# Kernel tuning notes

Measured on AMD Instinct MI355X. Metric: run time of the kernel, lower is better.

The kernel has to match this reference:

```python
import jax, jax.numpy as jnp
import numpy as np

D_MODEL = 1024
D_FF = 4096
NUM_HEADS = 16
HEAD_DIM = D_MODEL // NUM_HEADS
THETA = 10000.0
EPS = 1e-5


def _trunc_init(key, shape):
    fan_in, fan_out = shape
    sigma = (2.0 / (fan_in + fan_out)) ** 0.5
    return sigma * jax.random.truncated_normal(key, -3.0, 3.0, shape, dtype=jnp.float32)


def setup_inputs() -> dict:
    key = jax.random.key(0)
    ks = jax.random.split(key, 8)
    x = jax.random.normal(ks[0], (2, 2048, D_MODEL), dtype=jnp.float32)
    return {
        "x": x,
        "Wq": _trunc_init(ks[1], (D_MODEL, D_MODEL)),
        "Wk": _trunc_init(ks[2], (D_MODEL, D_MODEL)),
        "Wv": _trunc_init(ks[3], (D_MODEL, D_MODEL)),
        "Wo": _trunc_init(ks[4], (D_MODEL, D_MODEL)),
        "g1": jnp.ones((D_MODEL,), dtype=jnp.float32),
        "g2": jnp.ones((D_MODEL,), dtype=jnp.float32),
        "W1": _trunc_init(ks[5], (D_MODEL, D_FF)),
        "W2": _trunc_init(ks[6], (D_FF, D_MODEL)),
        "W3": _trunc_init(ks[7], (D_MODEL, D_FF)),
    }


def _rmsnorm(x, g):
    xf = x.astype(jnp.float32)
    rms = jnp.sqrt(jnp.mean(xf * xf, axis=-1, keepdims=True) + EPS)
    return (xf / rms * g).astype(x.dtype)


def _rope(x, cos, sin):
    # x: [B, H, S, Dh]; cos/sin: [S, Dh//2]
    x1 = x[..., 0::2]
    x2 = x[..., 1::2]
    o1 = x1 * cos - x2 * sin
    o2 = x2 * cos + x1 * sin
    return jnp.stack([o1, o2], axis=-1).reshape(x.shape)


def reference(x, Wq, Wk, Wv, Wo, g1, g2, W1, W2, W3):
    B, S, _ = x.shape
    # --- attention branch ---
    h = _rmsnorm(x, g1)
    def split_heads(t):
        return t.reshape(B, S, NUM_HEADS, HEAD_DIM).transpose(0, 2, 1, 3)
    Q = split_heads(h @ Wq)
    K = split_heads(h @ Wk)
    V = split_heads(h @ Wv)
    # RoPE
    powers = jnp.arange(0, HEAD_DIM, 2, dtype=jnp.float32) / HEAD_DIM
    inv_freq = 1.0 / (THETA ** powers)
    t = jnp.arange(S, dtype=jnp.float32)
    freqs = jnp.outer(t, inv_freq)  # [S, Dh//2]
    cos, sin = jnp.cos(freqs), jnp.sin(freqs)
    Q = _rope(Q, cos, sin)
    K = _rope(K, cos, sin)
    # scaled dot-product attention with causal mask
    scale = 1.0 / jnp.sqrt(jnp.float32(HEAD_DIM))
    scores = jnp.einsum('bhqd,bhkd->bhqk', Q, K) * scale
    causal = jnp.tril(jnp.ones((S, S), dtype=bool))
    scores = jnp.where(causal, scores, -jnp.inf)
    attn = jax.nn.softmax(scores, axis=-1)
    ctx = jnp.einsum('bhqk,bhkd->bhqd', attn, V)
    ctx = ctx.transpose(0, 2, 1, 3).reshape(B, S, D_MODEL)
    out1 = x + ctx @ Wo
    # --- FFN branch (SwiGLU) ---
    h2 = _rmsnorm(out1, g2)
    x1 = h2 @ W1
    x3 = h2 @ W3
    ffn = (x1 * jax.nn.sigmoid(x1) * x3) @ W2
    return out1 + ffn
```

## Files before the change

kernel.cpp:

```cpp
#include <hip/hip_runtime.h>
#include <math.h>

typedef unsigned short ushort_t;
typedef __attribute__((ext_vector_type(8))) short short8;
typedef __attribute__((ext_vector_type(4))) float f32x4;

#define MFMA16(a, b, c) __builtin_amdgcn_mfma_f32_16x16x32_bf16((a), (b), (c), 0, 0, 0)

static __device__ __forceinline__ float fast_exp2(float x) {
#if __has_builtin(__builtin_amdgcn_exp2f)
  return __builtin_amdgcn_exp2f(x);
#else
  return exp2f(x);
#endif
}

static __device__ __forceinline__ ushort_t f2bf(float f) {
  unsigned int u = __float_as_uint(f);
  u = u + 0x7FFFu + ((u >> 16) & 1u);
  return (ushort_t)(u >> 16);
}
static __device__ __forceinline__ ushort_t f2bf_trunc(float f) {
  return (ushort_t)(__float_as_uint(f) >> 16);
}
static __device__ __forceinline__ float bf2f(ushort_t s) {
  return __uint_as_float(((unsigned int)s) << 16);
}

static __device__ __forceinline__ void stage16(const ushort_t* g_perlane, char* l_uniform, int lane) {
#if __has_builtin(__builtin_amdgcn_global_load_lds)
  __builtin_amdgcn_global_load_lds((const __attribute__((address_space(1))) void*)g_perlane,
                                   (__attribute__((address_space(3))) void*)l_uniform, 16, 0, 0);
#else
  *(uint4*)(l_uniform + lane * 16) = *(const uint4*)g_perlane;
#endif
}

__global__ __launch_bounds__(256) void rmsnorm_k(const float* __restrict__ x,
                                                 const float* __restrict__ g,
                                                 ushort_t* __restrict__ o) {
  const int r = blockIdx.x, t = threadIdx.x;
  const float4 xv = ((const float4*)(x + (size_t)r * 1024))[t];
  float ss = xv.x * xv.x + xv.y * xv.y + xv.z * xv.z + xv.w * xv.w;
#pragma unroll
  for (int m = 32; m >= 1; m >>= 1) ss += __shfl_xor(ss, m);
  __shared__ float wp[4];
  if ((t & 63) == 0) wp[t >> 6] = ss;
  __syncthreads();
  const float inv = rsqrtf((wp[0] + wp[1] + wp[2] + wp[3]) * (1.f / 1024.f) + 1e-5f);
  const float4 gv = ((const float4*)g)[t];
  ushort4 ov = {f2bf(xv.x * inv * gv.x), f2bf(xv.y * inv * gv.y),
                f2bf(xv.z * inv * gv.z), f2bf(xv.w * inv * gv.w)};
  *(ushort4*)(o + (size_t)r * 1024 + t * 4) = ov;
}

__global__ __launch_bounds__(256) void transpose4_k(const float* __restrict__ s0,
                                                    const float* __restrict__ s1,
                                                    const float* __restrict__ s2,
                                                    const float* __restrict__ s3,
                                                    ushort_t* __restrict__ d0,
                                                    ushort_t* __restrict__ d1,
                                                    ushort_t* __restrict__ d2,
                                                    ushort_t* __restrict__ d3) {
  const int z = blockIdx.z;
  const float* in = (z == 0) ? s0 : (z == 1) ? s1 : (z == 2) ? s2 : s3;
  ushort_t* out = (z == 0) ? d0 : (z == 1) ? d1 : (z == 2) ? d2 : d3;
  __shared__ ushort_t Ts[64][72];
  const int t = threadIdx.x;
  const int c0 = blockIdx.x * 64, r0 = blockIdx.y * 64;
  const int lr = t >> 4, lc = (t & 15) * 4;
#pragma unroll
  for (int i = 0; i < 4; ++i) {
    const float4 v = *(const float4*)&in[(size_t)(r0 + lr + i * 16) * 1024 + c0 + lc];
    Ts[lr + i * 16][lc + 0] = f2bf(v.x);
    Ts[lr + i * 16][lc + 1] = f2bf(v.y);
    Ts[lr + i * 16][lc + 2] = f2bf(v.z);
    Ts[lr + i * 16][lc + 3] = f2bf(v.w);
  }
  __syncthreads();
  const int rr = (t & 15) * 4;
#pragma unroll
  for (int i = 0; i < 4; ++i) {
    const int cc = (t >> 4) + i * 16;
    ushort4 o = {Ts[rr + 0][cc], Ts[rr + 1][cc], Ts[rr + 2][cc], Ts[rr + 3][cc]};
    *(ushort4*)&out[(size_t)(c0 + cc) * 1024 + r0 + rr] = o;
  }
}

__global__ __launch_bounds__(256) void transpose3_k(const float* __restrict__ s0,
                                                    const float* __restrict__ s1,
                                                    const float* __restrict__ s2,
                                                    ushort_t* __restrict__ d01,
                                                    ushort_t* __restrict__ d2) {
  const int z = blockIdx.z;
  const float* in;
  ushort_t* out;
  int R, C, mode, c0, r0;
  if (z == 2) {
    in = s2; out = d2; R = 4096; C = 1024; mode = 0;
    const int flat = blockIdx.y * 64 + blockIdx.x;
    c0 = (flat & 15) * 64;
    r0 = (flat >> 4) * 64;
  } else {
    in = (z == 0) ? s0 : s1; out = d01; R = 1024; C = 4096; mode = (z == 0) ? 1 : 2;
    c0 = blockIdx.x * 64;
    r0 = blockIdx.y * 64;
  }
  __shared__ ushort_t Ts[64][72];
  const int t = threadIdx.x;
  const int lr = t >> 4, lc = (t & 15) * 4;
#pragma unroll
  for (int i = 0; i < 4; ++i) {
    const float4 v = *(const float4*)&in[(size_t)(r0 + lr + i * 16) * C + c0 + lc];
    Ts[lr + i * 16][lc + 0] = f2bf(v.x);
    Ts[lr + i * 16][lc + 1] = f2bf(v.y);
    Ts[lr + i * 16][lc + 2] = f2bf(v.z);
    Ts[lr + i * 16][lc + 3] = f2bf(v.w);
  }
  __syncthreads();
  const int rr = (t & 15) * 4;
#pragma unroll
  for (int i = 0; i < 4; ++i) {
    const int cc = (t >> 4) + i * 16;
    const int cg = c0 + cc;
    int orow;
    if (mode == 0)
      orow = cg;
    else
      orow = ((cg >> 7) << 8) + (((cg >> 4) & 7) << 5) + (cg & 15) + (mode == 2 ? 16 : 0);
    ushort4 o = {Ts[rr + 0][cc], Ts[rr + 1][cc], Ts[rr + 2][cc], Ts[rr + 3][cc]};
    *(ushort4*)&out[(size_t)orow * R + r0 + rr] = o;
  }
}

template <int FUSED>
__global__ __launch_bounds__(512, 2) void gemm256_k(const ushort_t* __restrict__ A,
                                                    const ushort_t* __restrict__ Bt,
                                                    ushort_t* __restrict__ C,
                                                    int N, int K) {
  __shared__ uint4 smem[131072 / 16];
  char* sm = (char*)smem;
  const int flat = blockIdx.y * gridDim.x + blockIdx.x;
  const int xcd = flat & 7;
  const int idx = flat >> 3;
  const int bx = (xcd & 3) * 8 + (idx & 7);
  const int by = (xcd >> 2) * 8 + (idx >> 3);
  const int t = threadIdx.x, lane = t & 63, w = t >> 6;
  const int g = lane >> 4, li = lane & 15;
  const int wr = w >> 2, wc = w & 3;
  const int nr0 = bx * 256, m0 = by * 256;
  const int wb4 = (t & 448) << 4;
  const int srow = t & 255;
  const int sg0 = t >> 8;
  const size_t rowA = (size_t)(m0 + srow) * K;
  const size_t rowB = (size_t)(nr0 + srow) * K;
  f32x4 acc[8][4] = {};
  const int nkt = K >> 5;

  auto stageA = [&](int kt) {
    char* dA = sm + (kt & 3) * 16384;
    const int k0 = kt << 5;
#pragma unroll
    for (int c = 0; c < 2; ++c)
      stage16(A + rowA + k0 + (c * 2 + sg0) * 8, dA + ((c * 512) << 4) + wb4, lane);
  };
  auto stageB = [&](int kt) {
    char* dB = sm + 65536 + (kt & 3) * 16384;
    const int k0 = kt << 5;
#pragma unroll
    for (int c = 0; c < 2; ++c)
      stage16(Bt + rowB + k0 + (c * 2 + sg0) * 8, dB + ((c * 512) << 4) + wb4, lane);
  };

  stageA(0); stageB(0); stageA(1); stageB(1);
  asm volatile("s_waitcnt vmcnt(4)" ::: "memory");
  __builtin_amdgcn_s_barrier();
  for (int kt = 0; kt < nkt; ++kt) {
    const char* sA = sm + (kt & 3) * 16384;
    const char* sB = sm + 65536 + (kt & 3) * 16384;
    const bool pf = (kt + 2 < nkt);
    short8 af0[4], bfr[4];
#pragma unroll
    for (int mi = 0; mi < 4; ++mi)
      af0[mi] = *(const short8*)(sA + ((g * 256 + wr * 128 + mi * 16 + li) << 4));
#pragma unroll
    for (int ni = 0; ni < 4; ++ni)
      bfr[ni] = *(const short8*)(sB + ((g * 256 + wc * 64 + ni * 16 + li) << 4));
    if (pf) stageA(kt + 2);
    __builtin_amdgcn_s_barrier();
    __builtin_amdgcn_s_setprio(1);
#pragma unroll
    for (int mi = 0; mi < 4; ++mi)
#pragma unroll
      for (int ni = 0; ni < 4; ++ni) acc[mi][ni] = MFMA16(af0[mi], bfr[ni], acc[mi][ni]);
    __builtin_amdgcn_s_setprio(0);
    __builtin_amdgcn_s_barrier();
    short8 af1[4];
#pragma unroll
    for (int mi = 0; mi < 4; ++mi)
      af1[mi] = *(const short8*)(sA + ((g * 256 + wr * 128 + (mi + 4) * 16 + li) << 4));
    if (pf) stageB(kt + 2);
    if (pf)
      asm volatile("s_waitcnt vmcnt(4)" ::: "memory");
    else if (kt + 1 < nkt)
      asm volatile("s_waitcnt vmcnt(0)" ::: "memory");
    __builtin_amdgcn_s_barrier();
    __builtin_amdgcn_s_setprio(1);
#pragma unroll
    for (int mi = 0; mi < 4; ++mi)
#pragma unroll
      for (int ni = 0; ni < 4; ++ni) acc[mi + 4][ni] = MFMA16(af1[mi], bfr[ni], acc[mi + 4][ni]);
    __builtin_amdgcn_s_setprio(0);
    __builtin_amdgcn_s_barrier();
  }
  if (FUSED == 0) {
#pragma unroll
    for (int mi = 0; mi < 8; ++mi)
#pragma unroll
      for (int ni = 0; ni < 4; ++ni)
#pragma unroll
        for (int r = 0; r < 4; ++r) {
          const int row = m0 + wr * 128 + mi * 16 + g * 4 + r;
          const int col = nr0 + wc * 64 + ni * 16 + li;
          C[(size_t)row * N + col] = f2bf(acc[mi][ni][r]);
        }
  } else {
#pragma unroll
    for (int mi = 0; mi < 8; ++mi)
#pragma unroll
      for (int p = 0; p < 2; ++p)
#pragma unroll
        for (int r = 0; r < 4; ++r) {
          const float v1 = acc[mi][2 * p][r];
          const float v3 = acc[mi][2 * p + 1][r];
          const float o = v1 / (1.f + __expf(-v1)) * v3;
          const int row = m0 + wr * 128 + mi * 16 + g * 4 + r;
          const int col = bx * 128 + wc * 32 + p * 16 + li;
          C[(size_t)row * N + col] = f2bf(o);
        }
  }
}

template <int MODE, int QKV2D>
__global__ __launch_bounds__(256) void gemm_k(const ushort_t* __restrict__ A,
                                              const ushort_t* __restrict__ Bt,
                                              const float* __restrict__ R,
                                              void* __restrict__ C,
                                              int N, int K) {
  __shared__ uint4 smem[49152 / 16];
  char* sm = (char*)smem;
  const int flat = blockIdx.y * gridDim.x + blockIdx.x;
  int bx, by;
  if (QKV2D) {
    const int xcd = flat & 7;
    const int idx = flat >> 3;
    bx = (xcd & 1) * 12 + idx % 12;
    by = (xcd >> 1) * 8 + idx / 12;
  } else {
    const int total = gridDim.x * gridDim.y;
    const int swz = (flat & 7) * (total >> 3) + (flat >> 3);
    bx = swz % gridDim.x;
    by = swz / gridDim.x;
  }
  const int t = threadIdx.x, lane = t & 63, w = t >> 6;
  const int g = lane >> 4, li = lane & 15;
  const int wr = w >> 1, wc = w & 1;
  const int n0 = bx * 128, m0 = by * 128;
  const int wb = t & 192;
  const int r0s = t & 127, g0s = (t >> 7) << 3;
  const size_t rowA = (size_t)(m0 + r0s) * K;
  const size_t rowB = (size_t)(n0 + r0s) * K;
  f32x4 acc[4][4] = {};
  const int nkt = K >> 5;

  auto stage_all = [&](int buf, int kt) {
    const int k0 = (kt << 5) + g0s;
    char* dA = sm + buf * 8192;
    char* dB = sm + 24576 + buf * 8192;
    stage16(A + rowA + k0, dA + (wb << 4), lane);
    stage16(A + rowA + k0 + 16, dA + ((256 + wb) << 4), lane);
    stage16(Bt + rowB + k0, dB + (wb << 4), lane);
    stage16(Bt + rowB + k0 + 16, dB + ((256 + wb) << 4), lane);
  };

  stage_all(0, 0);
  stage_all(1, 1);
  asm volatile("s_waitcnt vmcnt(4)" ::: "memory");
  __builtin_amdgcn_s_barrier();
  int b0 = 0;
  for (int kt = 0; kt < nkt; ++kt) {
    int bn = b0 + 2;
    if (bn >= 3) bn -= 3;
    if (kt + 2 < nkt) stage_all(bn, kt + 2);
    const char* smA = sm + b0 * 8192;
    const char* smB = sm + 24576 + b0 * 8192;
    short8 af[4], bfr[4];
#pragma unroll
    for (int mi = 0; mi < 4; ++mi)
      af[mi] = *(const short8*)(smA + ((g * 128 + wr * 64 + mi * 16 + li) << 4));
#pragma unroll
    for (int ni = 0; ni < 4; ++ni)
      bfr[ni] = *(const short8*)(smB + ((g * 128 + wc * 64 + ni * 16 + li) << 4));
    __builtin_amdgcn_s_setprio(1);
#pragma unroll
    for (int mi = 0; mi < 4; ++mi)
#pragma unroll
      for (int ni = 0; ni < 4; ++ni) acc[mi][ni] = MFMA16(af[mi], bfr[ni], acc[mi][ni]);
    __builtin_amdgcn_s_setprio(0);
    if (kt + 2 < nkt) {
      asm volatile("s_waitcnt vmcnt(4) lgkmcnt(0)" ::: "memory");
      __builtin_amdgcn_s_barrier();
    } else if (kt + 1 < nkt) {
      asm volatile("s_waitcnt vmcnt(0) lgkmcnt(0)" ::: "memory");
      __builtin_amdgcn_s_barrier();
    }
    ++b0;
    if (b0 == 3) b0 = 0;
  }
#pragma unroll
  for (int mi = 0; mi < 4; ++mi)
#pragma unroll
    for (int ni = 0; ni < 4; ++ni)
#pragma unroll
      for (int r = 0; r < 4; ++r) {
        const int row = m0 + wr * 64 + mi * 16 + g * 4 + r;
        const int col = n0 + wc * 64 + ni * 16 + li;
        const float v = acc[mi][ni][r];
        if (MODE == 1) {
          ((float*)C)[(size_t)row * N + col] = v + R[(size_t)row * N + col];
        } else if (MODE == 2) {
          const int sect = col >> 10;
          float ov = v;
          const float p = __shfl_xor(v, 1);
          if (sect < 2) {
            const float fi = (float)((col & 63) >> 1);
            const float fs = (float)(row & 2047);
            const float ang = fs * __expf(-fi * 0.28782313662425572f);
            float sn, cs;
            __sincosf(ang, &sn, &cs);
            const float scale = (sect == 0) ? 0.18033688011112042f : 1.0f;
            ov = ((li & 1) == 0) ? (v * cs - p * sn) * scale : (v * cs + p * sn) * scale;
          }
          ((ushort_t*)C)[(size_t)row * N + col] = f2bf(ov);
        } else {
          ((ushort_t*)C)[(size_t)row * N + col] = f2bf(v);
        }
      }
}

template <int MODE>
__global__ __launch_bounds__(256) void gemmbk64_k(const ushort_t* __restrict__ A,
                                                  const ushort_t* __restrict__ Bt,
                                                  const float* __restrict__ R,
                                                  void* __restrict__ C,
                                                  int N, int K) {
  __shared__ uint4 smem[98304 / 16];
  char* sm = (char*)smem;
  const int flat = blockIdx.y * gridDim.x + blockIdx.x;
  const int total = gridDim.x * gridDim.y;
  const int swz = (flat & 7) * (total >> 3) + (flat >> 3);
  const int bx = swz % gridDim.x, by = swz / gridDim.x;
  const int t = threadIdx.x, lane = t & 63, w = t >> 6;
  const int g = lane >> 4, li = lane & 15;
  const int wr = w >> 1, wc = w & 1;
  const int n0 = bx * 128, m0 = by * 128;
  const int wb = t & 192;
  const int r0s = t & 127, oc = t >> 7;
  const size_t rowA = (size_t)(m0 + r0s) * K;
  const size_t rowB = (size_t)(n0 + r0s) * K;
  f32x4 acc[4][4] = {};
  const int nkt = K >> 6;

  auto stageAh = [&](int buf, int kt) {
    const int k0 = kt << 6;
    char* dA = sm + buf * 16384;
#pragma unroll
    for (int c = 0; c < 4; ++c)
      stage16(A + rowA + k0 + (c * 2 + oc) * 8, dA + ((c * 256 + wb) << 4), lane);
  };
  auto stageBh = [&](int buf, int kt) {
    const int k0 = kt << 6;
    char* dB = sm + 49152 + buf * 16384;
#pragma unroll
    for (int c = 0; c < 4; ++c)
      stage16(Bt + rowB + k0 + (c * 2 + oc) * 8, dB + ((c * 256 + wb) << 4), lane);
  };

  stageAh(0, 0); stageBh(0, 0);
  stageAh(1, 1); stageBh(1, 1);
  asm volatile("s_waitcnt vmcnt(8)" ::: "memory");
  __builtin_amdgcn_s_barrier();
  int b0 = 0;
  for (int kt = 0; kt < nkt; ++kt) {
    int bn = b0 + 2;
    if (bn >= 3) bn -= 3;
    const bool pf = (kt + 2 < nkt);
    const char* smA = sm + b0 * 16384;
    const char* smB = sm + 49152 + b0 * 16384;
    short8 af0[4], bf0[4];
#pragma unroll
    for (int mi = 0; mi < 4; ++mi)
      af0[mi] = *(const short8*)(smA + ((g * 128 + wr * 64 + mi * 16 + li) << 4));
#pragma unroll
    for (int ni = 0; ni < 4; ++ni)
      bf0[ni] = *(const short8*)(smB + ((g * 128 + wc * 64 + ni * 16 + li) << 4));
    if (pf) stageAh(bn, kt + 2);
    __builtin_amdgcn_s_barrier();
    __builtin_amdgcn_s_setprio(1);
#pragma unroll
    for (int mi = 0; mi < 4; ++mi)
#pragma unroll
      for (int ni = 0; ni < 4; ++ni) acc[mi][ni] = MFMA16(af0[mi], bf0[ni], acc[mi][ni]);
    __builtin_amdgcn_s_setprio(0);
    __builtin_amdgcn_s_barrier();
    short8 af1[4], bf1[4];
#pragma unroll
    for (int mi = 0; mi < 4; ++mi)
      af1[mi] = *(const short8*)(smA + (((4 + g) * 128 + wr * 64 + mi * 16 + li) << 4));
#pragma unroll
    for (int ni = 0; ni < 4; ++ni)
      bf1[ni] = *(const short8*)(smB + (((4 + g) * 128 + wc * 64 + ni * 16 + li) << 4));
    if (pf) stageBh(bn, kt + 2);
    if (pf)
      asm volatile("s_waitcnt vmcnt(8) lgkmcnt(0)" ::: "memory");
    else if (kt + 1 < nkt)
      asm volatile("s_waitcnt vmcnt(0) lgkmcnt(0)" ::: "memory");
    __builtin_amdgcn_s_barrier();
    __builtin_amdgcn_s_setprio(1);
#pragma unroll
    for (int mi = 0; mi < 4; ++mi)
#pragma unroll
      for (int ni = 0; ni < 4; ++ni) acc[mi][ni] = MFMA16(af1[mi], bf1[ni], acc[mi][ni]);
    __builtin_amdgcn_s_setprio(0);
    __builtin_amdgcn_s_barrier();
    ++b0;
    if (b0 == 3) b0 = 0;
  }
#pragma unroll
  for (int mi = 0; mi < 4; ++mi)
#pragma unroll
    for (int ni = 0; ni < 4; ++ni)
#pragma unroll
      for (int r = 0; r < 4; ++r) {
        const int row = m0 + wr * 64 + mi * 16 + g * 4 + r;
        const int col = n0 + wc * 64 + ni * 16 + li;
        const float v = acc[mi][ni][r];
        if (MODE == 1)
          ((float*)C)[(size_t)row * N + col] = v + R[(size_t)row * N + col];
        else
          ((ushort_t*)C)[(size_t)row * N + col] = f2bf(v);
      }
}

__global__ __launch_bounds__(256) void attn_k(const ushort_t* __restrict__ qkv,
                                              ushort_t* __restrict__ ctx) {
  __shared__ uint4 smemv[32768 / 16];
  char* sm = (char*)smemv;
  const int bh = blockIdx.y;
  const int b = bh >> 4, h = bh & 15;
  const int t = threadIdx.x, lane = t & 63, w = t >> 6;
  const int g = lane >> 4, li = lane & 15;
  const int rowb = b * 2048;
  const size_t qbase = (size_t)rowb * 3072 + h * 64;
  const ushort_t* kptr = qkv + qbase + 1024;
  const ushort_t* vptr = qkv + qbase + 2048;
  const int sb = g * 20;

  const int vj = t & 63;
  const int vcol2 = 2 * (((vj >> 5) << 5) + (((vj >> 2) & 3) << 3) + (((vj >> 4) & 1) << 2) + (vj & 3));

  uint4 vr0, vr1;
  auto stageK = [&](int buf, int kt) {
    char* dst = sm + buf * 8192;
    const ushort_t* src = kptr + (size_t)kt * 64 * 3072 + (size_t)(t & 63) * 3072;
    stage16(src + (t >> 6) * 8, dst + ((t & 192) << 4), lane);
    stage16(src + ((t >> 6) + 4) * 8, dst + 4096 + ((t & 192) << 4), lane);
  };
  auto loadV = [&](int kt) {
    const ushort_t* src = vptr + (size_t)(kt * 64 + vj) * 3072 + w * 16;
    vr0 = *(const uint4*)src;
    vr1 = *(const uint4*)(src + 8);
  };
  auto writeV = [&](int buf) {
    char* dst = sm + 16384 + buf * 8192;
    ushort_t tmp[16];
    *(uint4*)tmp = vr0;
    *(uint4*)(tmp + 8) = vr1;
#pragma unroll
    for (int e = 0; e < 16; ++e) {
      const int dh = w * 16 + e;
      *(ushort_t*)(dst + dh * 128 + (vcol2 ^ ((dh & 7) << 4))) = tmp[e];
    }
  };

  for (int hv = 0; hv < 2; ++hv) {
    const int qt = (hv == 0) ? (31 - (int)blockIdx.x) : (int)blockIdx.x;
    const int q0 = qt * 64;

    short8 qa[2];
    {
      const int qrow = q0 + w * 16 + li;
      qa[0] = *(const short8*)(qkv + qbase + (size_t)qrow * 3072 + 8 * g);
      qa[1] = *(const short8*)(qkv + qbase + (size_t)qrow * 3072 + 32 + 8 * g);
    }
    f32x4 acc[4] = {};
    float mr = -INFINITY, lr = 0.f;

    stageK(0, 0);
    loadV(0);
    writeV(0);
    __syncthreads();
    int cur = 0;
    for (int kt = 0; kt <= qt; ++kt) {
      if (kt < qt) {
        stageK(cur ^ 1, kt + 1);
        loadV(kt + 1);
      }
      const char* Kf = sm + cur * 8192;
      const char* Vt = sm + 16384 + cur * 8192;
      f32x4 s[4];
      __builtin_amdgcn_s_setprio(1);
#pragma unroll
      for (int nt = 0; nt < 4; ++nt) {
        f32x4 z = {0.f, 0.f, 0.f, 0.f};
#pragma unroll
        for (int hh = 0; hh < 2; ++hh) {
          const short8 kf = *(const short8*)(Kf + (((hh * 4 + g) * 64 + nt * 16 + li) << 4));
          z = MFMA16(kf, qa[hh], z);
        }
        s[nt] = z;
      }
      __builtin_amdgcn_s_setprio(0);
      if (kt == qt) {
        const int qq = q0 + w * 16 + li;
#pragma unroll
        for (int nt = 0; nt < 4; ++nt)
#pragma unroll
          for (int r = 0; r < 4; ++r)
            if (kt * 64 + nt * 16 + g * 4 + r > qq) s[nt][r] = -INFINITY;
      }
      float pm = -INFINITY;
#pragma unroll
      for (int nt = 0; nt < 4; ++nt)
#pragma unroll
        for (int r = 0; r < 4; ++r) pm = fmaxf(pm, s[nt][r]);
      pm = fmaxf(pm, __shfl_xor(pm, 16));
      pm = fmaxf(pm, __shfl_xor(pm, 32));
      if (__any(pm > mr + 11.5f)) {
        const float nm = fmaxf(mr, pm);
        const float rs = fast_exp2(mr - nm);
        mr = nm;
        lr *= rs;
#pragma unroll
        for (int r = 0; r < 4; ++r) {
          const float rsb = __shfl(rs, sb + r);
#pragma unroll
          for (int dt = 0; dt < 4; ++dt) acc[dt][r] *= rsb;
        }
      }
      float ps = 0.f;
#pragma unroll
      for (int nt = 0; nt < 4; ++nt)
#pragma unroll
        for (int r = 0; r < 4; ++r) {
          s[nt][r] = fast_exp2(s[nt][r] - mr);
          ps += s[nt][r];
        }
      ps += __shfl_xor(ps, 16);
      ps += __shfl_xor(ps, 32);
      lr += ps;
      if (kt < qt) writeV(cur ^ 1);
      short8 pa[2];
#pragma unroll
      for (int m = 0; m < 2; ++m)
#pragma unroll
        for (int r = 0; r < 4; ++r) {
          pa[m][r] = (short)f2bf_trunc(s[2 * m][r]);
          pa[m][4 + r] = (short)f2bf_trunc(s[2 * m + 1][r]);
        }
      __builtin_amdgcn_s_setprio(1);
#pragma unroll
      for (int dt = 0; dt < 4; ++dt) {
        const int dh = dt * 16 + li;
#pragma unroll
        for (int m = 0; m < 2; ++m) {
          const short8 vb = *(const short8*)(Vt + dh * 128 + ((m * 64 + g * 16) ^ ((dh & 7) << 4)));
          acc[dt] = MFMA16(pa[m], vb, acc[dt]);
        }
      }
      __builtin_amdgcn_s_setprio(0);
      __syncthreads();
      cur ^= 1;
    }
#pragma unroll
    for (int r = 0; r < 4; ++r) {
      const float lrb = __shfl(lr, sb + r);
      const float inv = 1.f / lrb;
      const int row = rowb + q0 + w * 16 + g * 4 + r;
#pragma unroll
      for (int dt = 0; dt < 4; ++dt) {
        const int col = h * 64 + dt * 16 + li;
        ctx[(size_t)row * 1024 + col] = f2bf(acc[dt][r] * inv);
      }
    }
  }
}

extern "C" void kernel_launch(void* const* d_in, const int* in_sizes, int n_in,
                              void* d_out, int out_size, void* d_ws, size_t ws_size,
                              hipStream_t stream) {
  const float* x = (const float*)d_in[0];
  const float* Wq = (const float*)d_in[1];
  const float* Wk = (const float*)d_in[2];
  const float* Wv = (const float*)d_in[3];
  const float* Wo = (const float*)d_in[4];
  const float* g1 = (const float*)d_in[5];
  const float* g2 = (const float*)d_in[6];
  const float* W1 = (const float*)d_in[7];
  const float* W2 = (const float*)d_in[8];
  const float* W3 = (const float*)d_in[9];
  float* out = (float*)d_out;

  char* wsb = (char*)d_ws;
  ushort_t* hb = (ushort_t*)(wsb);
  ushort_t* qkv = (ushort_t*)(wsb + (8u << 20));
  ushort_t* ctx = (ushort_t*)(wsb + (32u << 20));
  ushort_t* x1b = (ushort_t*)(wsb + (8u << 20));
  ushort_t* wqkvT = (ushort_t*)(wsb + (72u << 20));
  ushort_t* woT = (ushort_t*)(wsb + (78u << 20));
  ushort_t* w13iT = (ushort_t*)(wsb + (80u << 20));
  ushort_t* w2T = (ushort_t*)(wsb + (96u << 20));

  transpose4_k<<<dim3(16, 16, 4), 256, 0, stream>>>(Wq, Wk, Wv, Wo, wqkvT,
                                                    wqkvT + 1024 * 1024,
                                                    wqkvT + 2 * 1024 * 1024, woT);
  transpose3_k<<<dim3(64, 16, 3), 256, 0, stream>>>(W1, W3, W2, w13iT, w2T);

  rmsnorm_k<<<4096, 256, 0, stream>>>(x, g1, hb);
  gemm_k<2, 1><<<dim3(24, 32), 256, 0, stream>>>(hb, wqkvT, nullptr, qkv, 3072, 1024);
  attn_k<<<dim3(16, 32), 256, 0, stream>>>(qkv, ctx);
  gemmbk64_k<1><<<dim3(8, 32), 256, 0, stream>>>(ctx, woT, x, out, 1024, 1024);
  rmsnorm_k<<<4096, 256, 0, stream>>>(out, g2, hb);
  gemm256_k<1><<<dim3(32, 16), 512, 0, stream>>>(hb, w13iT, x1b, 4096, 1024);
  gemmbk64_k<1><<<dim3(8, 32), 256, 0, stream>>>(x1b, w2T, out, out, 1024, 4096);
}
```

Measured before the change: 327.2 us.

## Fuse second RMSNorm into Wo GEMM epilogue and FFN GEMM via partial sums

Removes the standalone second rmsnorm kernel. The Wo projection epilogue now writes the residual output, an unnormalized bf16 copy, and per-row partial sums of squares. The FFN up-projection applies the rsqrt scale from those partials in its epilogue, and g2 is folded into the W1/W3 weights during the transpose. The W2 GEMM also gets a new XCD-aware 2D block swizzle. The cost is that the unnormalized activations are rounded to bf16 before scaling, which slightly changes the numerics.

```diff
diff --git a/kernel.cpp b/kernel.cpp
--- a/kernel.cpp
+++ b/kernel.cpp
@@ -90,6 +90,7 @@
 __global__ __launch_bounds__(256) void transpose3_k(const float* __restrict__ s0,
                                                     const float* __restrict__ s1,
                                                     const float* __restrict__ s2,
+                                                    const float* __restrict__ g2,
                                                     ushort_t* __restrict__ d01,
                                                     ushort_t* __restrict__ d2) {
   const int z = blockIdx.z;
@@ -111,11 +112,12 @@
   const int lr = t >> 4, lc = (t & 15) * 4;
 #pragma unroll
   for (int i = 0; i < 4; ++i) {
+    const float gg = (mode == 0) ? 1.0f : g2[r0 + lr + i * 16];
     const float4 v = *(const float4*)&in[(size_t)(r0 + lr + i * 16) * C + c0 + lc];
-    Ts[lr + i * 16][lc + 0] = f2bf(v.x);
-    Ts[lr + i * 16][lc + 1] = f2bf(v.y);
-    Ts[lr + i * 16][lc + 2] = f2bf(v.z);
-    Ts[lr + i * 16][lc + 3] = f2bf(v.w);
+    Ts[lr + i * 16][lc + 0] = f2bf(v.x * gg);
+    Ts[lr + i * 16][lc + 1] = f2bf(v.y * gg);
+    Ts[lr + i * 16][lc + 2] = f2bf(v.z * gg);
+    Ts[lr + i * 16][lc + 3] = f2bf(v.w * gg);
   }
   __syncthreads();
   const int rr = (t & 15) * 4;
@@ -137,6 +139,7 @@
 __global__ __launch_bounds__(512, 2) void gemm256_k(const ushort_t* __restrict__ A,
                                                     const ushort_t* __restrict__ Bt,
                                                     ushort_t* __restrict__ C,
+                                                    const float* __restrict__ P,
                                                     int N, int K) {
   __shared__ uint4 smem[131072 / 16];
   char* sm = (char*)smem;
@@ -228,16 +231,24 @@
 #pragma unroll
     for (int mi = 0; mi < 8; ++mi)
 #pragma unroll
-      for (int p = 0; p < 2; ++p)
-#pragma unroll
-        for (int r = 0; r < 4; ++r) {
-          const float v1 = acc[mi][2 * p][r];
-          const float v3 = acc[mi][2 * p + 1][r];
+      for (int r = 0; r < 4; ++r) {
+        const int row = m0 + wr * 128 + mi * 16 + g * 4 + r;
+        const float4 p0 = *(const float4*)(P + (size_t)row * 16);
+        const float4 p1 = *(const float4*)(P + (size_t)row * 16 + 4);
+        const float4 p2 = *(const float4*)(P + (size_t)row * 16 + 8);
+        const float4 p3 = *(const float4*)(P + (size_t)row * 16 + 12);
+        const float ssum = (p0.x + p0.y + p0.z + p0.w) + (p1.x + p1.y + p1.z + p1.w) +
+                           (p2.x + p2.y + p2.z + p2.w) + (p3.x + p3.y + p3.z + p3.w);
+        const float s = rsqrtf(ssum * (1.f / 1024.f) + 1e-5f);
+#pragma unroll
+        for (int p = 0; p < 2; ++p) {
+          const float v1 = acc[mi][2 * p][r] * s;
+          const float v3 = acc[mi][2 * p + 1][r] * s;
           const float o = v1 / (1.f + __expf(-v1)) * v3;
-          const int row = m0 + wr * 128 + mi * 16 + g * 4 + r;
           const int col = bx * 128 + wc * 32 + p * 16 + li;
           C[(size_t)row * N + col] = f2bf(o);
         }
+      }
   }
 }
 
@@ -348,18 +359,29 @@
       }
 }
 
-template <int MODE>
+template <int MODE, int SUP2D>
 __global__ __launch_bounds__(256) void gemmbk64_k(const ushort_t* __restrict__ A,
                                                   const ushort_t* __restrict__ Bt,
                                                   const float* __restrict__ R,
                                                   void* __restrict__ C,
+                                                  ushort_t* __restrict__ H,
+                                                  float* __restrict__ P,
                                                   int N, int K) {
   __shared__ uint4 smem[98304 / 16];
   char* sm = (char*)smem;
   const int flat = blockIdx.y * gridDim.x + blockIdx.x;
-  const int total = gridDim.x * gridDim.y;
-  const int swz = (flat & 7) * (total >> 3) + (flat >> 3);
-  const int bx = swz % gridDim.x, by = swz / gridDim.x;
+  int bx, by;
+  if (SUP2D) {
+    const int xcd = flat & 7;
+    const int idx = flat >> 3;
+    bx = (xcd & 3) * 2 + (idx & 1);
+    by = (xcd >> 2) * 16 + (idx >> 1);
+  } else {
+    const int total = gridDim.x * gridDim.y;
+    const int swz = (flat & 7) * (total >> 3) + (flat >> 3);
+    bx = swz % gridDim.x;
+    by = swz / gridDim.x;
+  }
   const int t = threadIdx.x, lane = t & 63, w = t >> 6;
   const int g = lane >> 4, li = lane & 15;
   const int wr = w >> 1, wc = w & 1;
@@ -436,20 +458,43 @@
     ++b0;
     if (b0 == 3) b0 = 0;
   }
-#pragma unroll
-  for (int mi = 0; mi < 4; ++mi)
-#pragma unroll
-    for (int ni = 0; ni < 4; ++ni)
+  if (MODE == 3) {
+#pragma unroll
+    for (int mi = 0; mi < 4; ++mi)
 #pragma unroll
       for (int r = 0; r < 4; ++r) {
         const int row = m0 + wr * 64 + mi * 16 + g * 4 + r;
-        const int col = n0 + wc * 64 + ni * 16 + li;
-        const float v = acc[mi][ni][r];
-        if (MODE == 1)
-          ((float*)C)[(size_t)row * N + col] = v + R[(size_t)row * N + col];
-        else
-          ((ushort_t*)C)[(size_t)row * N + col] = f2bf(v);
-      }
+        float ss = 0.f;
+#pragma unroll
+        for (int ni = 0; ni < 4; ++ni) {
+          const int col = n0 + wc * 64 + ni * 16 + li;
+          const float v = acc[mi][ni][r] + R[(size_t)row * N + col];
+          ((float*)C)[(size_t)row * N + col] = v;
+          H[(size_t)row * 1024 + col] = f2bf(v);
+          ss += v * v;
+        }
+        ss += __shfl_xor(ss, 1);
+        ss += __shfl_xor(ss, 2);
+        ss += __shfl_xor(ss, 4);
+        ss += __shfl_xor(ss, 8);
+        if (li == 0) P[(size_t)row * 16 + bx * 2 + wc] = ss;
+      }
+  } else {
+#pragma unroll
+    for (int mi = 0; mi < 4; ++mi)
+#pragma unroll
+      for (int ni = 0; ni < 4; ++ni)
+#pragma unroll
+        for (int r = 0; r < 4; ++r) {
+          const int row = m0 + wr * 64 + mi * 16 + g * 4 + r;
+          const int col = n0 + wc * 64 + ni * 16 + li;
+          const float v = acc[mi][ni][r];
+          if (MODE == 1)
+            ((float*)C)[(size_t)row * N + col] = v + R[(size_t)row * N + col];
+          else
+            ((ushort_t*)C)[(size_t)row * N + col] = f2bf(v);
+        }
+  }
 }
 
 __global__ __launch_bounds__(256) void attn_k(const ushort_t* __restrict__ qkv,
@@ -626,6 +671,7 @@
   ushort_t* qkv = (ushort_t*)(wsb + (8u << 20));
   ushort_t* ctx = (ushort_t*)(wsb + (32u << 20));
   ushort_t* x1b = (ushort_t*)(wsb + (8u << 20));
+  float* rmsP = (float*)(wsb + (40u << 20));
   ushort_t* wqkvT = (ushort_t*)(wsb + (72u << 20));
   ushort_t* woT = (ushort_t*)(wsb + (78u << 20));
   ushort_t* w13iT = (ushort_t*)(wsb + (80u << 20));
@@ -634,13 +680,12 @@
   transpose4_k<<<dim3(16, 16, 4), 256, 0, stream>>>(Wq, Wk, Wv, Wo, wqkvT,
                                                     wqkvT + 1024 * 1024,
                                                     wqkvT + 2 * 1024 * 1024, woT);
-  transpose3_k<<<dim3(64, 16, 3), 256, 0, stream>>>(W1, W3, W2, w13iT, w2T);
+  transpose3_k<<<dim3(64, 16, 3), 256, 0, stream>>>(W1, W3, W2, g2, w13iT, w2T);
 
   rmsnorm_k<<<4096, 256, 0, stream>>>(x, g1, hb);
   gemm_k<2, 1><<<dim3(24, 32), 256, 0, stream>>>(hb, wqkvT, nullptr, qkv, 3072, 1024);
   attn_k<<<dim3(16, 32), 256, 0, stream>>>(qkv, ctx);
-  gemmbk64_k<1><<<dim3(8, 32), 256, 0, stream>>>(ctx, woT, x, out, 1024, 1024);
-  rmsnorm_k<<<4096, 256, 0, stream>>>(out, g2, hb);
-  gemm256_k<1><<<dim3(32, 16), 512, 0, stream>>>(hb, w13iT, x1b, 4096, 1024);
-  gemmbk64_k<1><<<dim3(8, 32), 256, 0, stream>>>(x1b, w2T, out, out, 1024, 4096);
-}
+  gemmbk64_k<3, 0><<<dim3(8, 32), 256, 0, stream>>>(ctx, woT, x, out, hb, rmsP, 1024, 1024);
+  gemm256_k<1><<<dim3(32, 16), 512, 0, stream>>>(hb, w13iT, x1b, rmsP, 4096, 1024);
+  gemmbk64_k<1, 1><<<dim3(8, 32), 256, 0, stream>>>(x1b, w2T, out, out, nullptr, nullptr, 1024, 4096);
+}
```

Result: slower. 337.4 us (+3.1%).
